# Optimization experiments

Hardware: AMD Instinct MI355X
Metric: run time of the kernel (lower is better)

## Reference

```python
import jax, jax.numpy as jnp
import numpy as np

N_NODES = 100000
N_EDGES = 1600000
IN_C, HID_C, OUT_C, N_CLS = 64, 128, 64, 20


def setup_inputs() -> dict:
    key = jax.random.key(0)
    ks = jax.random.split(key, 8)
    s = lambda k, sh: jax.random.normal(k, sh, dtype=jnp.float32) * (1.0 / np.sqrt(sh[0]))
    return {
        "x": jax.random.normal(ks[0], (N_NODES, IN_C), dtype=jnp.float32),
        "edge_index": jax.random.randint(ks[1], (2, N_EDGES), 0, N_NODES, dtype=jnp.int64),
        "w_self1": s(ks[2], (IN_C, HID_C)),
        "w_neigh1": s(ks[3], (IN_C, HID_C)),
        "b1": jnp.zeros((HID_C,), dtype=jnp.float32),
        "w_self2": s(ks[4], (HID_C, OUT_C)),
        "w_neigh2": s(ks[5], (HID_C, OUT_C)),
        "b2": jnp.zeros((OUT_C,), dtype=jnp.float32),
        "wc": s(ks[6], (OUT_C, N_CLS)),
        "bc": jnp.zeros((N_CLS,), dtype=jnp.float32),
    }


def _sage_mean(feat, src, dst, deg_inv, w_self, w_neigh, b):
    # gather messages along edges, segment-sum at destinations, mean-normalize
    msg_sum = jax.ops.segment_sum(feat[src], dst, num_segments=N_NODES)  # [N, d]
    h_neigh = msg_sum * deg_inv[:, None]
    return feat @ w_self + h_neigh @ w_neigh + b


def reference(x, edge_index, w_self1, w_neigh1, b1, w_self2, w_neigh2, b2, wc, bc):
    src, dst = edge_index[0], edge_index[1]
    deg = jax.ops.segment_sum(jnp.ones((src.shape[0],), dtype=x.dtype), dst,
                              num_segments=N_NODES)
    deg_inv = 1.0 / jnp.maximum(deg, 1.0)  # zero-degree nodes -> 0 neighbor mean
    h = jax.nn.relu(_sage_mean(x, src, dst, deg_inv, w_self1, w_neigh1, b1))
    h = jax.nn.relu(_sage_mean(h, src, dst, deg_inv, w_self2, w_neigh2, b2))
    return h @ wc + bc
```

## Files before the change

### kernel.cpp

```cpp
#include <hip/hip_runtime.h>

#define N_NODES 100000
#define N_EDGES 1600000
#define IN_C    64
#define HID_C   128
#define OUT_C   64
#define N_CLS   20

#define BUCKETS 196
#define XSL     8
#define WCAP    2560
#define EPB     4096
#define CAPB    44

#define CVT_BLOCKS 3125

typedef __attribute__((ext_vector_type(8))) short short8;
typedef __attribute__((ext_vector_type(4))) float floatx4;

__device__ __forceinline__ unsigned short f2bf(float f) {
    union { float f; unsigned u; } v; v.f = f;
    unsigned r = v.u + 0x7FFFu + ((v.u >> 16) & 1u);
    return (unsigned short)(r >> 16);
}
__device__ __forceinline__ unsigned pk2(float lo, float hi) {
    return (unsigned)f2bf(lo) | ((unsigned)f2bf(hi) << 16);
}
__device__ __forceinline__ float bflo(unsigned w) { return __uint_as_float(w << 16); }
__device__ __forceinline__ float bfhi(unsigned w) { return __uint_as_float(w & 0xFFFF0000u); }

#define ACC8(v) do { \
    a0 += bflo((v).x); a1 += bfhi((v).x); a2 += bflo((v).y); a3 += bfhi((v).y); \
    a4 += bflo((v).z); a5 += bfhi((v).z); a6 += bflo((v).w); a7 += bfhi((v).w); } while (0)

__global__ __launch_bounds__(256) void prologue_kernel(
        const float* __restrict__ x,
        const float* __restrict__ ws1, const float* __restrict__ wn1,
        const float* __restrict__ ws2, const float* __restrict__ wn2,
        unsigned short* __restrict__ xb,
        unsigned short* __restrict__ wt1s, unsigned short* __restrict__ wt1n,
        unsigned short* __restrict__ wt2s, unsigned short* __restrict__ wt2n,
        int* __restrict__ bcnt)
{
    const int bid = blockIdx.x, tid = threadIdx.x;
    if (bid < CVT_BLOCKS) {
        int i = bid * 256 + tid;
        float4 a = ((const float4*)x)[(size_t)i * 2];
        float4 b = ((const float4*)x)[(size_t)i * 2 + 1];
        uint4 r;
        r.x = pk2(a.x, a.y); r.y = pk2(a.z, a.w);
        r.z = pk2(b.x, b.y); r.w = pk2(b.z, b.w);
        ((uint4*)xb)[i] = r;
    } else if (bid == CVT_BLOCKS) {
        for (int i = tid; i < BUCKETS * XSL; i += 256) bcnt[i] = 0;
    } else {
        int i = (bid - CVT_BLOCKS - 1) * 256 + tid;
        if (i < 8192) {
            int o = i >> 6, c = i & 63;
            wt1s[i] = f2bf(ws1[c * 128 + o]);
            wt1n[i] = f2bf(wn1[c * 128 + o]);
        } else if (i < 16384) {
            int j = i - 8192;
            int o = j >> 7, c = j & 127;
            wt2s[j] = f2bf(ws2[c * 64 + o]);
            wt2n[j] = f2bf(wn2[c * 64 + o]);
        }
    }
}

__global__ __launch_bounds__(256) void binA_kernel(
        const int* __restrict__ ei, int* __restrict__ bcnt,
        unsigned* __restrict__ bins)
{
    __shared__ unsigned lbins[BUCKETS * CAPB];
    __shared__ unsigned comp[EPB];
    __shared__ unsigned dsti[EPB];
    __shared__ int lcnt[BUCKETS], lofs[BUCKETS], gb[BUCKETS];
    __shared__ int sd[256];

    const int tid = threadIdx.x;
    const int xcd = blockIdx.x & (XSL - 1);
    const int e0  = blockIdx.x * EPB;

    for (int w = tid; w < BUCKETS; w += 256) lcnt[w] = 0;
    __syncthreads();

    for (int it = 0; it < EPB / 256; ++it) {
        int e = e0 + it * 256 + tid;
        if (e >= N_EDGES) break;
        int src = ei[e];
        int dst = ei[N_EDGES + e];
        int b = dst >> 9;
        unsigned pk = ((unsigned)(dst & 511) << 17) | (unsigned)src;
        int pos = atomicAdd(&lcnt[b], 1);
        if (pos < CAPB) {
            lbins[b * CAPB + pos] = pk;
        } else {
            int gp = atomicAdd(&bcnt[b * XSL + xcd], 1);
            if (gp < WCAP)
                bins[(unsigned)(b * XSL + xcd) * WCAP + gp] = pk;
        }
    }
    __syncthreads();

    int c = (tid < BUCKETS) ? min(lcnt[tid], CAPB) : 0;
    sd[tid] = c;
    __syncthreads();
    for (int off = 1; off < 256; off <<= 1) {
        int x = 0;
        if (tid >= off) x = sd[tid - off];
        __syncthreads();
        if (tid >= off) sd[tid] += x;
        __syncthreads();
    }
    if (tid < BUCKETS) lofs[tid] = sd[tid] - c;
    __syncthreads();
    const int T = sd[255];

    if (tid < BUCKETS) {
        int cw = min(lcnt[tid], CAPB);
        gb[tid] = (cw > 0) ? atomicAdd(&bcnt[tid * XSL + xcd], cw) : 0;
    }
    __syncthreads();

    if (tid < BUCKETS) {
        int cw = min(lcnt[tid], CAPB);
        int lo = lofs[tid];
        unsigned wb = (unsigned)(tid * XSL + xcd) * WCAP + (unsigned)gb[tid];
        for (int i = 0; i < cw; ++i) {
            comp[lo + i] = lbins[tid * CAPB + i];
            dsti[lo + i] = wb + i;
        }
    }
    __syncthreads();

    for (int i = tid; i < T; i += 256)
        bins[dsti[i]] = comp[i];
}

__global__ __launch_bounds__(256) void buildB_kernel(
        const int* __restrict__ bcnt, const unsigned* __restrict__ bins,
        int* __restrict__ row_ptr, int* __restrict__ sorted_src,
        float* __restrict__ dinv)
{
    __shared__ unsigned ent[16384];
    __shared__ int scnt[XSL], soff[XSL];
    __shared__ int cnt[512], lofs[512], cur[512];
    __shared__ int sd[256];
    __shared__ int gbase_s;

    const int b   = blockIdx.x;
    const int tid = threadIdx.x;
    const int node0 = b * 512;

    int part = 0;
    for (int w = tid; w < b * XSL; w += 256) part += min(bcnt[w], WCAP);
    sd[tid] = part;
    __syncthreads();
    for (int off = 128; off > 0; off >>= 1) {
        if (tid < off) sd[tid] += sd[tid + off];
        __syncthreads();
    }
    if (tid == 0) {
        gbase_s = sd[0];
        if (b == 0) row_ptr[N_NODES] = N_EDGES;
    }
    __syncthreads();

    if (tid < XSL) scnt[tid] = min(bcnt[b * XSL + tid], WCAP);
    { int i = tid; cnt[i] = 0; cnt[i + 256] = 0; }
    __syncthreads();
    if (tid == 0) {
        int acc = 0;
        for (int sl = 0; sl < XSL; ++sl) {
            soff[sl] = acc;
            acc += scnt[sl];
            if (acc > 16384) { scnt[sl] -= (acc - 16384); acc = 16384; }
        }
    }
    __syncthreads();

    for (int sl = 0; sl < XSL; ++sl) {
        int len = scnt[sl];
        const unsigned* seg = bins + (unsigned)(b * XSL + sl) * WCAP;
        int base = soff[sl];
        for (int i = tid; i < len; i += 256) {
            unsigned e = seg[i];
            ent[base + i] = e;
            atomicAdd((unsigned*)&cnt[e >> 17], 1u);
        }
    }
    __syncthreads();
    const int T = soff[XSL - 1] + scnt[XSL - 1];

    int a0 = cnt[2 * tid], a1 = cnt[2 * tid + 1];
    int s2 = a0 + a1;
    sd[tid] = s2;
    __syncthreads();
    for (int off = 1; off < 256; off <<= 1) {
        int x = 0;
        if (tid >= off) x = sd[tid - off];
        __syncthreads();
        if (tid >= off) sd[tid] += x;
        __syncthreads();
    }
    int excl = sd[tid] - s2;
    lofs[2 * tid]     = excl;
    lofs[2 * tid + 1] = excl + a0;
    cur[2 * tid]      = excl;
    cur[2 * tid + 1]  = excl + a0;
    __syncthreads();

    const int gbase = gbase_s;
    for (int j = tid; j < 512; j += 256) {
        int node = node0 + j;
        if (node < N_NODES) {
            row_ptr[node] = gbase + lofs[j];
            dinv[node] = 1.0f / (float)max(cnt[j], 1);
        }
    }
    for (int i = tid; i < T; i += 256) {
        unsigned e = ent[i];
        int dl = e >> 17;
        int p = atomicAdd((unsigned*)&cur[dl], 1u);
        sorted_src[gbase + p] = (int)(e & 0x1FFFFu);
    }
}

__global__ __launch_bounds__(256) void gather1_kernel(
        const int* __restrict__ row_ptr, const int* __restrict__ srcs,
        const unsigned short* __restrict__ featb,
        const float* __restrict__ dinv, unsigned short* __restrict__ aggb)
{
    int gid = blockIdx.x * 256 + threadIdx.x;
    int n = gid >> 3;
    int q = gid & 7;
    const uint4* f4 = (const uint4*)featb;
    float a0=0,a1=0,a2=0,a3=0,a4=0,a5=0,a6=0,a7=0;
    int beg = row_ptr[n];
    int end = row_ptr[n + 1];
    int e = beg;
    for (; e + 4 <= end; e += 4) {
        int s0 = srcs[e], s1 = srcs[e+1], s2 = srcs[e+2], s3 = srcs[e+3];
        uint4 v0 = f4[(size_t)s0 * 8 + q];
        uint4 v1 = f4[(size_t)s1 * 8 + q];
        uint4 v2 = f4[(size_t)s2 * 8 + q];
        uint4 v3 = f4[(size_t)s3 * 8 + q];
        ACC8(v0); ACC8(v1); ACC8(v2); ACC8(v3);
    }
    for (; e < end; ++e) {
        uint4 v = f4[(size_t)srcs[e] * 8 + q];
        ACC8(v);
    }
    float di = dinv[n];
    uint4 r;
    r.x = pk2(a0 * di, a1 * di);
    r.y = pk2(a2 * di, a3 * di);
    r.z = pk2(a4 * di, a5 * di);
    r.w = pk2(a6 * di, a7 * di);
    ((uint4*)aggb)[(size_t)n * 8 + q] = r;
}

__global__ __launch_bounds__(256, 8) void mlp1_kernel(
        const unsigned short* __restrict__ xb,
        const unsigned short* __restrict__ aggb,
        const unsigned short* __restrict__ wt1s,
        const unsigned short* __restrict__ wt1n,
        const float* __restrict__ b1,
        const unsigned short* __restrict__ wt2n,
        const unsigned short* __restrict__ wt2s,
        const float* __restrict__ b2,
        unsigned short* __restrict__ t2b,
        unsigned short* __restrict__ s2b)
{
    __shared__ unsigned short sbuf[32 * 136];

    const int tid = threadIdx.x;
    const int node0 = blockIdx.x * 32;

    const int lane  = tid & 63;
    const int wv    = tid >> 6;
    const int quad  = lane >> 4;
    const int col   = lane & 15;
    const int nrow  = (wv & 1) * 16 + col;
    const int mhalf = wv >> 1;
    const int nl = node0 + nrow;

    {
        const short8 bs0 = *(const short8*)(xb   + (size_t)nl * 64 +      quad * 8);
        const short8 bs1 = *(const short8*)(xb   + (size_t)nl * 64 + 32 + quad * 8);
        const short8 bn0 = *(const short8*)(aggb + (size_t)nl * 64 +      quad * 8);
        const short8 bn1 = *(const short8*)(aggb + (size_t)nl * 64 + 32 + quad * 8);

#pragma unroll
        for (int mt = 0; mt < 4; ++mt) {
            int mb = mhalf * 4 + mt;
            int m = mb * 16 + col;
            const short8 as0 = *(const short8*)(wt1s + (size_t)m * 64 +      quad * 8);
            const short8 as1 = *(const short8*)(wt1s + (size_t)m * 64 + 32 + quad * 8);
            const short8 an0 = *(const short8*)(wt1n + (size_t)m * 64 +      quad * 8);
            const short8 an1 = *(const short8*)(wt1n + (size_t)m * 64 + 32 + quad * 8);
            floatx4 acc = {0.f, 0.f, 0.f, 0.f};
            acc = __builtin_amdgcn_mfma_f32_16x16x32_bf16(as0, bs0, acc, 0, 0, 0);
            acc = __builtin_amdgcn_mfma_f32_16x16x32_bf16(as1, bs1, acc, 0, 0, 0);
            acc = __builtin_amdgcn_mfma_f32_16x16x32_bf16(an0, bn0, acc, 0, 0, 0);
            acc = __builtin_amdgcn_mfma_f32_16x16x32_bf16(an1, bn1, acc, 0, 0, 0);
            int och = mb * 16 + quad * 4;
            float4 bv = *(const float4*)(b1 + och);
            ushort4 r;
            r.x = f2bf(fmaxf(acc[0] + bv.x, 0.f));
            r.y = f2bf(fmaxf(acc[1] + bv.y, 0.f));
            r.z = f2bf(fmaxf(acc[2] + bv.z, 0.f));
            r.w = f2bf(fmaxf(acc[3] + bv.w, 0.f));
            *(ushort4*)(sbuf + nrow * 136 + och) = r;
        }
    }
    __syncthreads();

    {
        short8 bfr[4];
#pragma unroll
        for (int kc = 0; kc < 4; ++kc)
            bfr[kc] = *(const short8*)(sbuf + nrow * 136 + kc * 32 + quad * 8);

#pragma unroll
        for (int mt = 0; mt < 2; ++mt) {
            int mb = mhalf * 2 + mt;
            int m = mb * 16 + col;
            floatx4 at = {0.f, 0.f, 0.f, 0.f};
            floatx4 as = {0.f, 0.f, 0.f, 0.f};
#pragma unroll
            for (int kc = 0; kc < 4; ++kc) {
                const short8 an = *(const short8*)(wt2n + (size_t)m * 128 + kc * 32 + quad * 8);
                const short8 aw = *(const short8*)(wt2s + (size_t)m * 128 + kc * 32 + quad * 8);
                at = __builtin_amdgcn_mfma_f32_16x16x32_bf16(an, bfr[kc], at, 0, 0, 0);
                as = __builtin_amdgcn_mfma_f32_16x16x32_bf16(aw, bfr[kc], as, 0, 0, 0);
            }
            int och = mb * 16 + quad * 4;
            ushort4 rt;
            rt.x = f2bf(at[0]); rt.y = f2bf(at[1]);
            rt.z = f2bf(at[2]); rt.w = f2bf(at[3]);
            *(ushort4*)(t2b + (size_t)nl * 64 + och) = rt;
            float4 bv = *(const float4*)(b2 + och);
            ushort4 rs;
            rs.x = f2bf(as[0] + bv.x); rs.y = f2bf(as[1] + bv.y);
            rs.z = f2bf(as[2] + bv.z); rs.w = f2bf(as[3] + bv.w);
            *(ushort4*)(s2b + (size_t)nl * 64 + och) = rs;
        }
    }
}

__global__ __launch_bounds__(256, 8) void fused2_kernel(
        const int* __restrict__ row_ptr, const int* __restrict__ srcs,
        const unsigned short* __restrict__ t2b,
        const unsigned short* __restrict__ s2b,
        const float* __restrict__ dinv,
        const float* __restrict__ wc,
        const float* __restrict__ bc,
        float* __restrict__ out)
{
    __shared__ float hs[32][68];

    const int tid = threadIdx.x;
    const int node0 = blockIdx.x * 32;

    {
        const int q  = tid & 7;
        const int np = tid >> 3;
        const int n = node0 + np;
        const uint4* f4 = (const uint4*)t2b;
        float a0=0,a1=0,a2=0,a3=0,a4=0,a5=0,a6=0,a7=0;
        int beg = row_ptr[n];
        int end = row_ptr[n + 1];
        int e = beg;
        for (; e + 4 <= end; e += 4) {
            int s0 = srcs[e], s1 = srcs[e+1], s2 = srcs[e+2], s3 = srcs[e+3];
            uint4 v0 = f4[(size_t)s0 * 8 + q];
            uint4 v1 = f4[(size_t)s1 * 8 + q];
            uint4 v2 = f4[(size_t)s2 * 8 + q];
            uint4 v3 = f4[(size_t)s3 * 8 + q];
            ACC8(v0); ACC8(v1); ACC8(v2); ACC8(v3);
        }
        for (; e < end; ++e) {
            uint4 v = f4[(size_t)srcs[e] * 8 + q];
            ACC8(v);
        }
        float di = dinv[n];
        uint4 sv = *(const uint4*)(s2b + (size_t)n * 64 + q * 8);
        float* d = hs[np] + q * 8;
        d[0] = fmaxf(a0 * di + bflo(sv.x), 0.f);
        d[1] = fmaxf(a1 * di + bfhi(sv.x), 0.f);
        d[2] = fmaxf(a2 * di + bflo(sv.y), 0.f);
        d[3] = fmaxf(a3 * di + bfhi(sv.y), 0.f);
        d[4] = fmaxf(a4 * di + bflo(sv.z), 0.f);
        d[5] = fmaxf(a5 * di + bfhi(sv.z), 0.f);
        d[6] = fmaxf(a6 * di + bflo(sv.w), 0.f);
        d[7] = fmaxf(a7 * di + bfhi(sv.w), 0.f);
    }
    __syncthreads();

    for (int o = tid; o < 32 * N_CLS; o += 256) {
        int n = o / N_CLS, cls = o % N_CLS;
        float s = bc[cls];
#pragma unroll
        for (int k = 0; k < 64; ++k) s += hs[n][k] * wc[k * N_CLS + cls];
        out[(size_t)(node0 + n) * N_CLS + cls] = s;
    }
}


extern "C" void kernel_launch(void* const* d_in, const int* in_sizes, int n_in,
                              void* d_out, int out_size, void* d_ws, size_t ws_size,
                              hipStream_t stream)
{
    const float* x        = (const float*)d_in[0];
    const int*   ei       = (const int*)  d_in[1];
    const float* w_self1  = (const float*)d_in[2];
    const float* w_neigh1 = (const float*)d_in[3];
    const float* b1       = (const float*)d_in[4];
    const float* w_self2  = (const float*)d_in[5];
    const float* w_neigh2 = (const float*)d_in[6];
    const float* b2       = (const float*)d_in[7];
    const float* wc       = (const float*)d_in[8];
    const float* bc       = (const float*)d_in[9];
    float* out = (float*)d_out;

    const size_t N = N_NODES;
    int*      bcnt    = (int*)d_ws;
    int*      row_ptr = bcnt + BUCKETS * XSL + 8;
    unsigned* bins    = (unsigned*)(row_ptr + N + 8);
    int*      s_src   = (int*)(bins + BUCKETS * XSL * WCAP);
    float*    dinv    = (float*)(s_src + N_EDGES);
    unsigned short* xb    = (unsigned short*)(dinv + N);
    unsigned short* agg1b = xb + 64 * N;
    unsigned short* t2b   = agg1b + 64 * N;
    unsigned short* s2b   = t2b + 64 * N;
    unsigned short* wt1s  = s2b + 64 * N;
    unsigned short* wt1n  = wt1s + 8192;
    unsigned short* wt2s  = wt1n + 8192;
    unsigned short* wt2n  = wt2s + 8192;

    const int PB  = CVT_BLOCKS + 1 + 64;
    const int EB2 = (N_EDGES + EPB - 1) / EPB;
    const int GB  = (N_NODES * 8) / 256;
    const int MB32 = (N_NODES + 31) / 32;

    prologue_kernel<<<PB, 256, 0, stream>>>(x, w_self1, w_neigh1, w_self2,
                                            w_neigh2, xb, wt1s, wt1n, wt2s,
                                            wt2n, bcnt);
    binA_kernel<<<EB2, 256, 0, stream>>>(ei, bcnt, bins);
    buildB_kernel<<<BUCKETS, 256, 0, stream>>>(bcnt, bins, row_ptr, s_src, dinv);
    gather1_kernel<<<GB, 256, 0, stream>>>(row_ptr, s_src, xb, dinv, agg1b);
    mlp1_kernel<<<MB32, 256, 0, stream>>>(xb, agg1b, wt1s, wt1n, b1,
                                          wt2n, wt2s, b2, t2b, s2b);
    fused2_kernel<<<MB32, 256, 0, stream>>>(row_ptr, s_src, t2b, s2b, dinv,
                                            wc, bc, out);
}
```

Before: 305.5 us.

## Make mlp1 persistent with register-resident weights and prefetched node tiles

```diff
diff --git a/kernel.cpp b/kernel.cpp
--- a/kernel.cpp
+++ b/kernel.cpp
@@ -14,6 +14,8 @@
 #define CAPB    44
 
 #define CVT_BLOCKS 3125
+#define NTILES    3125
+#define MLP_GRID  512
 
 typedef __attribute__((ext_vector_type(8))) short short8;
 typedef __attribute__((ext_vector_type(4))) float floatx4;
@@ -261,7 +263,7 @@
     ((uint4*)aggb)[(size_t)n * 8 + q] = r;
 }
 
-__global__ __launch_bounds__(256, 8) void mlp1_kernel(
+__global__ __launch_bounds__(256, 2) void mlp1_kernel(
         const unsigned short* __restrict__ xb,
         const unsigned short* __restrict__ aggb,
         const unsigned short* __restrict__ wt1s,
@@ -275,78 +277,113 @@
 {
     __shared__ unsigned short sbuf[32 * 136];
 
-    const int tid = threadIdx.x;
-    const int node0 = blockIdx.x * 32;
-
-    const int lane  = tid & 63;
-    const int wv    = tid >> 6;
-    const int quad  = lane >> 4;
-    const int col   = lane & 15;
-    const int nrow  = (wv & 1) * 16 + col;
+    const int tid  = threadIdx.x;
+    const int lane = tid & 63;
+    const int wv   = tid >> 6;
+    const int quad = lane >> 4;
+    const int col  = lane & 15;
+    const int nrow = (wv & 1) * 16 + col;
     const int mhalf = wv >> 1;
-    const int nl = node0 + nrow;
-
+
+    short8 wBs0[4], wBs1[4], wBn0[4], wBn1[4];
+#pragma unroll
+    for (int mt = 0; mt < 4; ++mt) {
+        size_t m = (size_t)((mhalf * 4 + mt) * 16 + col);
+        wBs0[mt] = *(const short8*)(wt1s + m * 64 +      quad * 8);
+        wBs1[mt] = *(const short8*)(wt1s + m * 64 + 32 + quad * 8);
+        wBn0[mt] = *(const short8*)(wt1n + m * 64 +      quad * 8);
+        wBn1[mt] = *(const short8*)(wt1n + m * 64 + 32 + quad * 8);
+    }
+    short8 wCt[2][4], wCs[2][4];
+#pragma unroll
+    for (int mt = 0; mt < 2; ++mt) {
+        size_t m = (size_t)((mhalf * 2 + mt) * 16 + col);
+#pragma unroll
+        for (int kc = 0; kc < 4; ++kc) {
+            wCt[mt][kc] = *(const short8*)(wt2n + m * 128 + kc * 32 + quad * 8);
+            wCs[mt][kc] = *(const short8*)(wt2s + m * 128 + kc * 32 + quad * 8);
+        }
+    }
+    float4 bv1[4];
+#pragma unroll
+    for (int mt = 0; mt < 4; ++mt)
+        bv1[mt] = *(const float4*)(b1 + (mhalf * 4 + mt) * 16 + quad * 4);
+    float4 bv2[2];
+#pragma unroll
+    for (int mt = 0; mt < 2; ++mt)
+        bv2[mt] = *(const float4*)(b2 + (mhalf * 2 + mt) * 16 + quad * 4);
+
+    int tile = blockIdx.x;
+    short8 bs0, bs1, bn0, bn1;
     {
-        const short8 bs0 = *(const short8*)(xb   + (size_t)nl * 64 +      quad * 8);
-        const short8 bs1 = *(const short8*)(xb   + (size_t)nl * 64 + 32 + quad * 8);
-        const short8 bn0 = *(const short8*)(aggb + (size_t)nl * 64 +      quad * 8);
-        const short8 bn1 = *(const short8*)(aggb + (size_t)nl * 64 + 32 + quad * 8);
-
+        const int nl = tile * 32 + nrow;
+        bs0 = *(const short8*)(xb   + (size_t)nl * 64 +      quad * 8);
+        bs1 = *(const short8*)(xb   + (size_t)nl * 64 + 32 + quad * 8);
+        bn0 = *(const short8*)(aggb + (size_t)nl * 64 +      quad * 8);
+        bn1 = *(const short8*)(aggb + (size_t)nl * 64 + 32 + quad * 8);
+    }
+
+    while (tile < NTILES) {
+        const int nl = tile * 32 + nrow;
+        const int next = tile + MLP_GRID;
+
+        floatx4 accB[4];
 #pragma unroll
         for (int mt = 0; mt < 4; ++mt) {
-            int mb = mhalf * 4 + mt;
-            int m = mb * 16 + col;
-            const short8 as0 = *(const short8*)(wt1s + (size_t)m * 64 +      quad * 8);
-            const short8 as1 = *(const short8*)(wt1s + (size_t)m * 64 + 32 + quad * 8);
-            const short8 an0 = *(const short8*)(wt1n + (size_t)m * 64 +      quad * 8);
-            const short8 an1 = *(const short8*)(wt1n + (size_t)m * 64 + 32 + quad * 8);
             floatx4 acc = {0.f, 0.f, 0.f, 0.f};
-            acc = __builtin_amdgcn_mfma_f32_16x16x32_bf16(as0, bs0, acc, 0, 0, 0);
-            acc = __builtin_amdgcn_mfma_f32_16x16x32_bf16(as1, bs1, acc, 0, 0, 0);
-            acc = __builtin_amdgcn_mfma_f32_16x16x32_bf16(an0, bn0, acc, 0, 0, 0);
-            acc = __builtin_amdgcn_mfma_f32_16x16x32_bf16(an1, bn1, acc, 0, 0, 0);
-            int och = mb * 16 + quad * 4;
-            float4 bv = *(const float4*)(b1 + och);
+            acc = __builtin_amdgcn_mfma_f32_16x16x32_bf16(wBs0[mt], bs0, acc, 0, 0, 0);
+            acc = __builtin_amdgcn_mfma_f32_16x16x32_bf16(wBs1[mt], bs1, acc, 0, 0, 0);
+            acc = __builtin_amdgcn_mfma_f32_16x16x32_bf16(wBn0[mt], bn0, acc, 0, 0, 0);
+            acc = __builtin_amdgcn_mfma_f32_16x16x32_bf16(wBn1[mt], bn1, acc, 0, 0, 0);
+            accB[mt] = acc;
+        }
+
+        if (next < NTILES) {
+            const int nn = next * 32 + nrow;
+            bs0 = *(const short8*)(xb   + (size_t)nn * 64 +      quad * 8);
+            bs1 = *(const short8*)(xb   + (size_t)nn * 64 + 32 + quad * 8);
+            bn0 = *(const short8*)(aggb + (size_t)nn * 64 +      quad * 8);
+            bn1 = *(const short8*)(aggb + (size_t)nn * 64 + 32 + quad * 8);
+        }
+
+        __syncthreads();
+#pragma unroll
+        for (int mt = 0; mt < 4; ++mt) {
+            int och = (mhalf * 4 + mt) * 16 + quad * 4;
             ushort4 r;
-            r.x = f2bf(fmaxf(acc[0] + bv.x, 0.f));
-            r.y = f2bf(fmaxf(acc[1] + bv.y, 0.f));
-            r.z = f2bf(fmaxf(acc[2] + bv.z, 0.f));
-            r.w = f2bf(fmaxf(acc[3] + bv.w, 0.f));
+            r.x = f2bf(fmaxf(accB[mt][0] + bv1[mt].x, 0.f));
+            r.y = f2bf(fmaxf(accB[mt][1] + bv1[mt].y, 0.f));
+            r.z = f2bf(fmaxf(accB[mt][2] + bv1[mt].z, 0.f));
+            r.w = f2bf(fmaxf(accB[mt][3] + bv1[mt].w, 0.f));
             *(ushort4*)(sbuf + nrow * 136 + och) = r;
         }
-    }
-    __syncthreads();
-
-    {
+        __syncthreads();
+
         short8 bfr[4];
 #pragma unroll
         for (int kc = 0; kc < 4; ++kc)
             bfr[kc] = *(const short8*)(sbuf + nrow * 136 + kc * 32 + quad * 8);
-
 #pragma unroll
         for (int mt = 0; mt < 2; ++mt) {
-            int mb = mhalf * 2 + mt;
-            int m = mb * 16 + col;
             floatx4 at = {0.f, 0.f, 0.f, 0.f};
             floatx4 as = {0.f, 0.f, 0.f, 0.f};
 #pragma unroll
             for (int kc = 0; kc < 4; ++kc) {
-                const short8 an = *(const short8*)(wt2n + (size_t)m * 128 + kc * 32 + quad * 8);
-                const short8 aw = *(const short8*)(wt2s + (size_t)m * 128 + kc * 32 + quad * 8);
-                at = __builtin_amdgcn_mfma_f32_16x16x32_bf16(an, bfr[kc], at, 0, 0, 0);
-                as = __builtin_amdgcn_mfma_f32_16x16x32_bf16(aw, bfr[kc], as, 0, 0, 0);
+                at = __builtin_amdgcn_mfma_f32_16x16x32_bf16(wCt[mt][kc], bfr[kc], at, 0, 0, 0);
+                as = __builtin_amdgcn_mfma_f32_16x16x32_bf16(wCs[mt][kc], bfr[kc], as, 0, 0, 0);
             }
-            int och = mb * 16 + quad * 4;
+            int och = (mhalf * 2 + mt) * 16 + quad * 4;
             ushort4 rt;
             rt.x = f2bf(at[0]); rt.y = f2bf(at[1]);
             rt.z = f2bf(at[2]); rt.w = f2bf(at[3]);
             *(ushort4*)(t2b + (size_t)nl * 64 + och) = rt;
-            float4 bv = *(const float4*)(b2 + och);
             ushort4 rs;
-            rs.x = f2bf(as[0] + bv.x); rs.y = f2bf(as[1] + bv.y);
-            rs.z = f2bf(as[2] + bv.z); rs.w = f2bf(as[3] + bv.w);
+            rs.x = f2bf(as[0] + bv2[mt].x); rs.y = f2bf(as[1] + bv2[mt].y);
+            rs.z = f2bf(as[2] + bv2[mt].z); rs.w = f2bf(as[3] + bv2[mt].w);
             *(ushort4*)(s2b + (size_t)nl * 64 + och) = rs;
         }
+
+        tile = next;
     }
 }
 
@@ -451,8 +488,8 @@
     binA_kernel<<<EB2, 256, 0, stream>>>(ei, bcnt, bins);
     buildB_kernel<<<BUCKETS, 256, 0, stream>>>(bcnt, bins, row_ptr, s_src, dinv);
     gather1_kernel<<<GB, 256, 0, stream>>>(row_ptr, s_src, xb, dinv, agg1b);
-    mlp1_kernel<<<MB32, 256, 0, stream>>>(xb, agg1b, wt1s, wt1n, b1,
-                                          wt2n, wt2s, b2, t2b, s2b);
+    mlp1_kernel<<<MLP_GRID, 256, 0, stream>>>(xb, agg1b, wt1s, wt1n, b1,
+                                              wt2n, wt2s, b2, t2b, s2b);
     fused2_kernel<<<MB32, 256, 0, stream>>>(row_ptr, s_src, t2b, s2b, dinv,
                                             wc, bc, out);
 }
```

Result: faster. 263.7 us (-13.7%).
